# Kernel tuning notes

Measured on AMD Instinct MI355X. Metric: run time of the kernel, lower is better.

Reference implementation:

```python
import jax, jax.numpy as jnp
import numpy as np
import math

N_HEAD = 16
STRIDE = 128
C = 8


def _sparse_causal_mask(q_len, k_len):
    # Mirrors LingLongAttention._sparse_causal_mask (static, host-side numpy).
    cols = np.arange(k_len)
    rows = np.arange(k_len)[:, None]
    strided = (cols % STRIDE) >= (STRIDE - C)          # last C cols of each stride block
    local = (cols[None, :] // STRIDE) == (rows // STRIDE)  # same stride block as query
    causal = cols[None, :] <= rows
    layout = (strided[None, :] | local) & causal       # [k_len, k_len]
    return jnp.asarray(layout[k_len - q_len:])         # [q_len, k_len]


def setup_inputs() -> dict:
    key = jax.random.key(0)
    k1, k2, k3 = jax.random.split(key, 3)
    B, S, E = 2, 2048, 1024
    return {
        "hidden_states": jax.random.normal(k1, (B, S, E), dtype=jnp.float32),
        "W_attn": jax.random.normal(k2, (E, 3 * E), dtype=jnp.float32) * 0.02,
        "b_attn": jnp.zeros((3 * E,), dtype=jnp.float32),
        "W_proj": jax.random.normal(k3, (E, E), dtype=jnp.float32) * 0.02,
        "b_proj": jnp.zeros((E,), dtype=jnp.float32),
    }


def reference(hidden_states, W_attn, b_attn, W_proj, b_proj):
    B, S, E = hidden_states.shape
    H = N_HEAD
    D = E // H
    # Conv1D: x @ W + b, then split into q,k,v
    qkv = hidden_states @ W_attn + b_attn                 # [B,S,3E]
    q, k, v = jnp.split(qkv, 3, axis=-1)
    split = lambda t: t.reshape(B, S, H, D).transpose(0, 2, 1, 3)  # [B,H,S,D]
    q, k, v = split(q), split(k), split(v)
    scale = jnp.asarray(1.0 / math.sqrt(D), dtype=q.dtype)
    scores = jnp.einsum("bhqd,bhkd->bhqk", q, k) * scale  # [B,H,S,S]
    mask = _sparse_causal_mask(S, S)[None, None]          # [1,1,S,S]
    mask_value = jnp.asarray(jnp.finfo(scores.dtype).min, dtype=scores.dtype)
    scores = jnp.where(mask, scores, mask_value)
    attn = jax.nn.softmax(scores, axis=-1)
    out = jnp.einsum("bhqk,bhkd->bhqd", attn, v)          # [B,H,S,D]
    out = out.transpose(0, 2, 1, 3).reshape(B, S, E)      # merge heads
    return out @ W_proj + b_proj
```

## Files before the change

kernel.cpp:

```cpp
#include <hip/hip_runtime.h>
#include <hip/hip_bf16.h>
#include <stdint.h>

typedef unsigned short u16;
typedef uint32_t u32;
typedef short s16x8 __attribute__((ext_vector_type(8)));
typedef float f32x4 __attribute__((ext_vector_type(4)));

#define SDIM 2048
#define EDIM 1024

static __device__ __forceinline__ float b2f(u16 v) {
    union { float f; u32 u; } c; c.u = ((u32)v) << 16; return c.f;
}
static __device__ __forceinline__ u16 f2b(float f) {
    union { float f; u32 u; } c; c.f = f;
    u32 u = c.u;
    u32 r = (u + 0x7FFFu + ((u >> 16) & 1u)) >> 16;
    return (u16)r;
}
static __device__ __forceinline__ void gll16(const u16* g, u16* l) {
    __builtin_amdgcn_global_load_lds(
        (const __attribute__((address_space(1))) void*)g,
        (__attribute__((address_space(3))) void*)l, 16, 0, 0);
}

static __device__ __forceinline__ int sniff_bf16(const u16* __restrict__ x) {
    u16 v = x[(threadIdx.x & 63) * 2];
    int e = (v >> 7) & 0xFF;
    unsigned long long m = __ballot(e >= 90 && e <= 144);
    return __popcll(m) >= 48;
}

__global__ __launch_bounds__(256) void k_prep(
    const void* __restrict__ X, const void* __restrict__ Wa,
    const void* __restrict__ Wp, u16* __restrict__ Xb,
    u16* __restrict__ WtA, u16* __restrict__ WtP) {
    int f = sniff_bf16((const u16*)X);
    int z = blockIdx.z;
    int t = threadIdx.x;
    if (z == 2) {
        if (f) return;
        const float* s = (const float*)X;
        int bid = blockIdx.y * 48 + blockIdx.x;
        for (int c = bid; c < 2048; c += 768) {
            long i = ((long)c * 256 + t) * 8;
            u16 o[8];
            for (int j = 0; j < 8; ++j) o[j] = f2b(s[i + j]);
            *(uint4*)&Xb[i] = *(uint4*)o;
        }
        return;
    }
    if (z == 1 && blockIdx.x >= 16) return;
    const void* src = z ? Wp : Wa;
    u16* dst = z ? WtP : WtA;
    int Nsrc = z ? 1024 : 3072;
    int n0 = blockIdx.x * 64, k0 = blockIdx.y * 64;
    __shared__ u16 L[64 * 72];
    int r = t >> 2, c0 = (t & 3) * 16;
    u16 val[16];
    if (f) {
        const u16* s = (const u16*)src + (size_t)(k0 + r) * Nsrc + n0 + c0;
        *(uint4*)&val[0] = *(const uint4*)s;
        *(uint4*)&val[8] = *(const uint4*)(s + 8);
    } else {
        const float* s = (const float*)src + (size_t)(k0 + r) * Nsrc + n0 + c0;
        for (int j = 0; j < 16; ++j) val[j] = f2b(s[j]);
    }
    for (int j = 0; j < 16; ++j) L[(c0 + j) * 72 + r] = val[j];
    __syncthreads();
    uint4 o0 = *(const uint4*)&L[r * 72 + c0];
    uint4 o1 = *(const uint4*)&L[r * 72 + c0 + 8];
    u16* d = dst + (size_t)(n0 + r) * 1024 + k0 + c0;
    *(uint4*)d = o0;
    *(uint4*)(d + 8) = o1;
}

__global__ __launch_bounds__(256) void k_gemm1(
    const u16* __restrict__ Xraw, const u16* __restrict__ Xb,
    const u16* __restrict__ Bt, const void* __restrict__ bias,
    u16* __restrict__ C) {
    const int K = 1024, N = 3072;
    __shared__ u16 As[128 * 64];
    __shared__ u16 Bs[128 * 64];
    int f = sniff_bf16(Xraw);
    const u16* A = f ? Xraw : Xb;
    int t = threadIdx.x, wave = t >> 6, lane = t & 63;
    int m0 = blockIdx.y * 128, n0 = blockIdx.x * 128;
    int wm = (wave >> 1) * 64, wn = (wave & 1) * 64;
    int lm = lane & 15, lk = (lane >> 4) * 8;
    int sr = t >> 2, sc = (t & 3) * 8;
    const u16* Ap = A + (size_t)(m0 + sr) * K + sc;
    const u16* Bp = Bt + (size_t)(n0 + sr) * K + sc;
    u16* Asw = As + wave * 512;
    u16* Bsw = Bs + wave * 512;

    f32x4 acc[4][4];
    f32x4 z = {0.f, 0.f, 0.f, 0.f};
    for (int mi = 0; mi < 4; ++mi)
        for (int ni = 0; ni < 4; ++ni) acc[mi][ni] = z;

    for (int k0 = 0; k0 < K; k0 += 64) {
        gll16(Ap + k0, Asw);
        gll16(Ap + (size_t)64 * K + k0, Asw + 2048);
        gll16(Ap + k0 + 32, Asw + 4096);
        gll16(Ap + (size_t)64 * K + k0 + 32, Asw + 6144);
        gll16(Bp + k0, Bsw);
        gll16(Bp + (size_t)64 * K + k0, Bsw + 2048);
        gll16(Bp + k0 + 32, Bsw + 4096);
        gll16(Bp + (size_t)64 * K + k0 + 32, Bsw + 6144);
        __syncthreads();
        for (int kh = 0; kh < 2; ++kh) {
            const u16* Ab = As + kh * 4096;
            const u16* Bb = Bs + kh * 4096;
            s16x8 af[4], bfr[4];
            for (int mi = 0; mi < 4; ++mi)
                af[mi] = *(const s16x8*)&Ab[(wm + mi * 16 + lm) * 32 + lk];
            for (int ni = 0; ni < 4; ++ni)
                bfr[ni] = *(const s16x8*)&Bb[(wn + ni * 16 + lm) * 32 + lk];
            for (int mi = 0; mi < 4; ++mi)
                for (int ni = 0; ni < 4; ++ni)
                    acc[mi][ni] = __builtin_amdgcn_mfma_f32_16x16x32_bf16(
                        af[mi], bfr[ni], acc[mi][ni], 0, 0, 0);
        }
        __syncthreads();
    }

    int cn = lane & 15, cr = (lane >> 4) * 4;
    for (int ni = 0; ni < 4; ++ni) {
        int gn = n0 + wn + ni * 16 + cn;
        float bb = f ? b2f(((const u16*)bias)[gn]) : ((const float*)bias)[gn];
        for (int mi = 0; mi < 4; ++mi)
            for (int r = 0; r < 4; ++r) {
                int gm = m0 + wm + mi * 16 + cr + r;
                C[(size_t)gm * N + gn] = f2b(acc[mi][ni][r] + bb);
            }
    }
}

__global__ __launch_bounds__(256) void k_gemm2(
    const u16* __restrict__ Xraw, const u16* __restrict__ A,
    const u16* __restrict__ Bt, const void* __restrict__ bias,
    u16* __restrict__ Cb, float* __restrict__ Cf) {
    const int K = 1024, N = 1024;
    __shared__ u16 As[64 * 64];
    __shared__ u16 Bs[128 * 64];
    int f = sniff_bf16(Xraw);
    int t = threadIdx.x, wave = t >> 6, lane = t & 63;
    int m0 = blockIdx.y * 64, n0 = blockIdx.x * 128;
    int wm = (wave >> 1) * 32, wn = (wave & 1) * 64;
    int lm = lane & 15, lk = (lane >> 4) * 8;
    int sr = t >> 2, sc = (t & 3) * 8;
    const u16* Ap = A + (size_t)(m0 + sr) * K + sc;
    const u16* Bp = Bt + (size_t)(n0 + sr) * K + sc;
    u16* Asw = As + wave * 512;
    u16* Bsw = Bs + wave * 512;

    f32x4 acc[2][4];
    f32x4 z = {0.f, 0.f, 0.f, 0.f};
    for (int mi = 0; mi < 2; ++mi)
        for (int ni = 0; ni < 4; ++ni) acc[mi][ni] = z;

    for (int k0 = 0; k0 < K; k0 += 64) {
        gll16(Ap + k0, Asw);
        gll16(Ap + k0 + 32, Asw + 2048);
        gll16(Bp + k0, Bsw);
        gll16(Bp + (size_t)64 * K + k0, Bsw + 2048);
        gll16(Bp + k0 + 32, Bsw + 4096);
        gll16(Bp + (size_t)64 * K + k0 + 32, Bsw + 6144);
        __syncthreads();
        for (int kh = 0; kh < 2; ++kh) {
            const u16* Ab = As + kh * 2048;
            const u16* Bb = Bs + kh * 4096;
            s16x8 af[2], bfr[4];
            for (int mi = 0; mi < 2; ++mi)
                af[mi] = *(const s16x8*)&Ab[(wm + mi * 16 + lm) * 32 + lk];
            for (int ni = 0; ni < 4; ++ni)
                bfr[ni] = *(const s16x8*)&Bb[(wn + ni * 16 + lm) * 32 + lk];
            for (int mi = 0; mi < 2; ++mi)
                for (int ni = 0; ni < 4; ++ni)
                    acc[mi][ni] = __builtin_amdgcn_mfma_f32_16x16x32_bf16(
                        af[mi], bfr[ni], acc[mi][ni], 0, 0, 0);
        }
        __syncthreads();
    }

    int store_f32 = (f == 0);
    int cn = lane & 15, cr = (lane >> 4) * 4;
    for (int ni = 0; ni < 4; ++ni) {
        int gn = n0 + wn + ni * 16 + cn;
        float bb = f ? b2f(((const u16*)bias)[gn]) : ((const float*)bias)[gn];
        for (int mi = 0; mi < 2; ++mi)
            for (int r = 0; r < 4; ++r) {
                int gm = m0 + wm + mi * 16 + cr + r;
                float v = acc[mi][ni][r] + bb;
                size_t o = (size_t)gm * N + gn;
                if (store_f32) Cf[o] = v;
                else           Cb[o] = f2b(v);
            }
    }
}

#define VP 264
#define PP 264
__global__ __launch_bounds__(256) void k_attn3(const u16* __restrict__ QKV,
                                               u16* __restrict__ AO) {
    int bx = blockIdx.x, h = blockIdx.y, b = blockIdx.z;
    int qb = bx >> 1, sb = bx & 1;
    int t = threadIdx.x, lane = t & 63, wave = t >> 6;
    int lm = lane & 15, q4 = lane >> 4;
    int nstr = qb << 3;
    int nk = nstr + (sb << 6) + 64;
    int r0 = (qb << 7) + (sb << 6);

    __shared__ char smem[79872];
    u16* Vts = (u16*)smem;
    u16* Qs  = (u16*)(smem + 33792);
    u16* Ks  = (u16*)(smem + 33792 + 9216);
    u16* Ps  = (u16*)(smem + 33792);

    const u16* base = QKV + (size_t)b * SDIM * 3072;

    for (int c = t; c < 512; c += 256) {
        int r = c >> 3, d0 = (c & 7) << 3;
        *(uint4*)&Qs[r * 72 + d0] =
            *(const uint4*)(base + (size_t)(r0 + r) * 3072 + h * 64 + d0);
    }
    uint4 zz = {0u, 0u, 0u, 0u};
    for (int c = t; c < 2048; c += 256) {
        int i = c >> 3, d0 = (c & 7) << 3;
        uint4 kv = zz;
        if (i < nk) {
            int key = (i < nstr) ? (((i >> 3) << 7) + 120 + (i & 7))
                                 : ((qb << 7) + (i - nstr));
            kv = *(const uint4*)(base + (size_t)key * 3072 + 1024 + h * 64 + d0);
        }
        *(uint4*)&Ks[i * 72 + d0] = kv;
    }
    {
        int i0 = (t & 31) * 8, d0 = (t >> 5) * 8;
        u16 m8[8][8];
        for (int r = 0; r < 8; ++r) {
            int i = i0 + r;
            uint4 vv = zz;
            if (i < nk) {
                int key = (i < nstr) ? (((i >> 3) << 7) + 120 + (i & 7))
                                     : ((qb << 7) + (i - nstr));
                vv = *(const uint4*)(base + (size_t)key * 3072 + 2048 + h * 64 + d0);
            }
            *(uint4*)m8[r] = vv;
        }
        for (int j = 0; j < 8; ++j) {
            u16 o[8];
            for (int r = 0; r < 8; ++r) o[r] = m8[r][j];
            *(uint4*)&Vts[(d0 + j) * VP + i0] = *(uint4*)o;
        }
    }
    __syncthreads();

    f32x4 acc[16];
    f32x4 z4 = {0.f, 0.f, 0.f, 0.f};
    for (int ni = 0; ni < 16; ++ni) acc[ni] = z4;
    s16x8 af0 = *(const s16x8*)&Qs[(wave * 16 + lm) * 72 + q4 * 8];
    s16x8 af1 = *(const s16x8*)&Qs[(wave * 16 + lm) * 72 + 32 + q4 * 8];
    for (int ni = 0; ni < 16; ++ni) {
        s16x8 bf0 = *(const s16x8*)&Ks[(ni * 16 + lm) * 72 + q4 * 8];
        s16x8 bf1 = *(const s16x8*)&Ks[(ni * 16 + lm) * 72 + 32 + q4 * 8];
        acc[ni] = __builtin_amdgcn_mfma_f32_16x16x32_bf16(af0, bf0, acc[ni], 0, 0, 0);
        acc[ni] = __builtin_amdgcn_mfma_f32_16x16x32_bf16(af1, bf1, acc[ni], 0, 0, 0);
    }
    __syncthreads();

    float mx[4] = {-3e38f, -3e38f, -3e38f, -3e38f};
    for (int ni = 0; ni < 16; ++ni) {
        int i = ni * 16 + lm;
        for (int reg = 0; reg < 4; ++reg) {
            int rl = (sb << 6) + wave * 16 + q4 * 4 + reg;
            bool valid = (i < nstr) || ((i - nstr) <= rl);
            float v = valid ? acc[ni][reg] * 0.125f : -3e38f;
            acc[ni][reg] = v;
            mx[reg] = fmaxf(mx[reg], v);
        }
    }
    for (int reg = 0; reg < 4; ++reg)
        for (int off = 1; off < 16; off <<= 1)
            mx[reg] = fmaxf(mx[reg], __shfl_xor(mx[reg], off, 64));
    float sm[4] = {0.f, 0.f, 0.f, 0.f};
    for (int ni = 0; ni < 16; ++ni)
        for (int reg = 0; reg < 4; ++reg) {
            float e = __expf(acc[ni][reg] - mx[reg]);
            acc[ni][reg] = e;
            sm[reg] += e;
        }
    for (int reg = 0; reg < 4; ++reg)
        for (int off = 1; off < 16; off <<= 1)
            sm[reg] += __shfl_xor(sm[reg], off, 64);
    float inv[4];
    for (int reg = 0; reg < 4; ++reg) inv[reg] = 1.f / sm[reg];

    for (int ni = 0; ni < 16; ++ni) {
        int i = ni * 16 + lm;
        for (int reg = 0; reg < 4; ++reg)
            Ps[(wave * 16 + q4 * 4 + reg) * PP + i] = f2b(acc[ni][reg]);
    }
    __syncthreads();

    f32x4 acc2[4];
    for (int ni2 = 0; ni2 < 4; ++ni2) acc2[ni2] = z4;
    for (int k0 = 0; k0 < 256; k0 += 32) {
        s16x8 pf = *(const s16x8*)&Ps[(wave * 16 + lm) * PP + k0 + q4 * 8];
        for (int ni2 = 0; ni2 < 4; ++ni2) {
            s16x8 vf = *(const s16x8*)&Vts[(ni2 * 16 + lm) * VP + k0 + q4 * 8];
            acc2[ni2] = __builtin_amdgcn_mfma_f32_16x16x32_bf16(pf, vf, acc2[ni2], 0, 0, 0);
        }
    }
    int srow = r0 + wave * 16 + q4 * 4;
    for (int ni2 = 0; ni2 < 4; ++ni2)
        for (int reg = 0; reg < 4; ++reg) {
            size_t o = ((size_t)(b * SDIM + srow + reg)) * EDIM + h * 64 + ni2 * 16 + lm;
            AO[o] = f2b(acc2[ni2][reg] * inv[reg]);
        }
}

extern "C" void kernel_launch(void* const* d_in, const int* in_sizes, int n_in,
                              void* d_out, int out_size, void* d_ws, size_t ws_size,
                              hipStream_t stream) {
    const void* X  = d_in[0];
    const void* Wa = d_in[1];
    const void* ba = d_in[2];
    const void* Wp = d_in[3];
    const void* bp = d_in[4];

    char* w = (char*)d_ws;
    u16* Xb   = (u16*)(w);
    u16* WtA  = (u16*)(w + 8388608);
    u16* WtP  = (u16*)(w + 14680064);
    u16* QKV  = (u16*)(w + 16777216);
    u16* AO   = (u16*)(w + 41943040);

    k_prep<<<dim3(48, 16, 3), 256, 0, stream>>>(X, Wa, Wp, Xb, WtA, WtP);
    k_gemm1<<<dim3(24, 32), 256, 0, stream>>>((const u16*)X, Xb, WtA, ba, QKV);
    k_attn3<<<dim3(32, 16, 2), 256, 0, stream>>>(QKV, AO);
    k_gemm2<<<dim3(8, 64), 256, 0, stream>>>((const u16*)X, AO, WtP, bp,
                                             (u16*)d_out, (float*)d_out);
}
```

Baseline: 169.6 us.

## Double-buffer A tiles in LDS and load B fragments directly from global in GEMMs

Both projection GEMMs now double-buffer the A tile in shared memory and prefetch the next k-slice while the current one is computed. This leaves one barrier per iteration instead of two. The B operand is no longer staged through LDS; each wave reads its MFMA fragments straight from global memory into registers. This removes the B staging and LDS traffic, but B is now fetched redundantly by the two waves that share a column range. The direct global loads also sit in the critical path with no prefetch distance, and they raise register pressure.

```diff
diff --git a/kernel.cpp b/kernel.cpp
--- a/kernel.cpp
+++ b/kernel.cpp
@@ -81,8 +81,7 @@
     const u16* __restrict__ Bt, const void* __restrict__ bias,
     u16* __restrict__ C) {
     const int K = 1024, N = 3072;
-    __shared__ u16 As[128 * 64];
-    __shared__ u16 Bs[128 * 64];
+    __shared__ u16 As[2 * 8192];
     int f = sniff_bf16(Xraw);
     const u16* A = f ? Xraw : Xb;
     int t = threadIdx.x, wave = t >> 6, lane = t & 63;
@@ -91,37 +90,44 @@
     int lm = lane & 15, lk = (lane >> 4) * 8;
     int sr = t >> 2, sc = (t & 3) * 8;
     const u16* Ap = A + (size_t)(m0 + sr) * K + sc;
-    const u16* Bp = Bt + (size_t)(n0 + sr) * K + sc;
-    u16* Asw = As + wave * 512;
-    u16* Bsw = Bs + wave * 512;
+    const u16* Bl = Bt + (size_t)(n0 + wn + lm) * K + lk;
+    u16* Asw0 = As + wave * 512;
 
     f32x4 acc[4][4];
     f32x4 z = {0.f, 0.f, 0.f, 0.f};
     for (int mi = 0; mi < 4; ++mi)
         for (int ni = 0; ni < 4; ++ni) acc[mi][ni] = z;
 
-    for (int k0 = 0; k0 < K; k0 += 64) {
-        gll16(Ap + k0, Asw);
-        gll16(Ap + (size_t)64 * K + k0, Asw + 2048);
-        gll16(Ap + k0 + 32, Asw + 4096);
-        gll16(Ap + (size_t)64 * K + k0 + 32, Asw + 6144);
-        gll16(Bp + k0, Bsw);
-        gll16(Bp + (size_t)64 * K + k0, Bsw + 2048);
-        gll16(Bp + k0 + 32, Bsw + 4096);
-        gll16(Bp + (size_t)64 * K + k0 + 32, Bsw + 6144);
-        __syncthreads();
+    gll16(Ap, Asw0);
+    gll16(Ap + (size_t)64 * K, Asw0 + 2048);
+    gll16(Ap + 32, Asw0 + 4096);
+    gll16(Ap + (size_t)64 * K + 32, Asw0 + 6144);
+    __syncthreads();
+
+    for (int it = 0; it < 16; ++it) {
+        int k0 = it * 64;
+        const u16* cur = As + (it & 1) * 8192;
+        if (it < 15) {
+            u16* nxt = As + ((it + 1) & 1) * 8192 + wave * 512;
+            int kn = k0 + 64;
+            gll16(Ap + kn, nxt);
+            gll16(Ap + (size_t)64 * K + kn, nxt + 2048);
+            gll16(Ap + kn + 32, nxt + 4096);
+            gll16(Ap + (size_t)64 * K + kn + 32, nxt + 6144);
+        }
+        s16x8 bfr[2][4];
+        for (int kh = 0; kh < 2; ++kh)
+            for (int ni = 0; ni < 4; ++ni)
+                bfr[kh][ni] = *(const s16x8*)(Bl + (size_t)(ni * 16) * K + k0 + kh * 32);
         for (int kh = 0; kh < 2; ++kh) {
-            const u16* Ab = As + kh * 4096;
-            const u16* Bb = Bs + kh * 4096;
-            s16x8 af[4], bfr[4];
+            const u16* Ab = cur + kh * 4096;
+            s16x8 af[4];
             for (int mi = 0; mi < 4; ++mi)
                 af[mi] = *(const s16x8*)&Ab[(wm + mi * 16 + lm) * 32 + lk];
-            for (int ni = 0; ni < 4; ++ni)
-                bfr[ni] = *(const s16x8*)&Bb[(wn + ni * 16 + lm) * 32 + lk];
             for (int mi = 0; mi < 4; ++mi)
                 for (int ni = 0; ni < 4; ++ni)
                     acc[mi][ni] = __builtin_amdgcn_mfma_f32_16x16x32_bf16(
-                        af[mi], bfr[ni], acc[mi][ni], 0, 0, 0);
+                        af[mi], bfr[kh][ni], acc[mi][ni], 0, 0, 0);
         }
         __syncthreads();
     }
@@ -143,8 +149,7 @@
     const u16* __restrict__ Bt, const void* __restrict__ bias,
     u16* __restrict__ Cb, float* __restrict__ Cf) {
     const int K = 1024, N = 1024;
-    __shared__ u16 As[64 * 64];
-    __shared__ u16 Bs[128 * 64];
+    __shared__ u16 As[2 * 4096];
     int f = sniff_bf16(Xraw);
     int t = threadIdx.x, wave = t >> 6, lane = t & 63;
     int m0 = blockIdx.y * 64, n0 = blockIdx.x * 128;
@@ -152,35 +157,40 @@
     int lm = lane & 15, lk = (lane >> 4) * 8;
     int sr = t >> 2, sc = (t & 3) * 8;
     const u16* Ap = A + (size_t)(m0 + sr) * K + sc;
-    const u16* Bp = Bt + (size_t)(n0 + sr) * K + sc;
-    u16* Asw = As + wave * 512;
-    u16* Bsw = Bs + wave * 512;
+    const u16* Bl = Bt + (size_t)(n0 + wn + lm) * K + lk;
+    u16* Asw0 = As + wave * 512;
 
     f32x4 acc[2][4];
     f32x4 z = {0.f, 0.f, 0.f, 0.f};
     for (int mi = 0; mi < 2; ++mi)
         for (int ni = 0; ni < 4; ++ni) acc[mi][ni] = z;
 
-    for (int k0 = 0; k0 < K; k0 += 64) {
-        gll16(Ap + k0, Asw);
-        gll16(Ap + k0 + 32, Asw + 2048);
-        gll16(Bp + k0, Bsw);
-        gll16(Bp + (size_t)64 * K + k0, Bsw + 2048);
-        gll16(Bp + k0 + 32, Bsw + 4096);
-        gll16(Bp + (size_t)64 * K + k0 + 32, Bsw + 6144);
-        __syncthreads();
+    gll16(Ap, Asw0);
+    gll16(Ap + 32, Asw0 + 2048);
+    __syncthreads();
+
+    for (int it = 0; it < 16; ++it) {
+        int k0 = it * 64;
+        const u16* cur = As + (it & 1) * 4096;
+        if (it < 15) {
+            u16* nxt = As + ((it + 1) & 1) * 4096 + wave * 512;
+            int kn = k0 + 64;
+            gll16(Ap + kn, nxt);
+            gll16(Ap + kn + 32, nxt + 2048);
+        }
+        s16x8 bfr[2][4];
+        for (int kh = 0; kh < 2; ++kh)
+            for (int ni = 0; ni < 4; ++ni)
+                bfr[kh][ni] = *(const s16x8*)(Bl + (size_t)(ni * 16) * K + k0 + kh * 32);
         for (int kh = 0; kh < 2; ++kh) {
-            const u16* Ab = As + kh * 2048;
-            const u16* Bb = Bs + kh * 4096;
-            s16x8 af[2], bfr[4];
+            const u16* Ab = cur + kh * 2048;
+            s16x8 af[2];
             for (int mi = 0; mi < 2; ++mi)
                 af[mi] = *(const s16x8*)&Ab[(wm + mi * 16 + lm) * 32 + lk];
-            for (int ni = 0; ni < 4; ++ni)
-                bfr[ni] = *(const s16x8*)&Bb[(wn + ni * 16 + lm) * 32 + lk];
             for (int mi = 0; mi < 2; ++mi)
                 for (int ni = 0; ni < 4; ++ni)
                     acc[mi][ni] = __builtin_amdgcn_mfma_f32_16x16x32_bf16(
-                        af[mi], bfr[ni], acc[mi][ni], 0, 0, 0);
+                        af[mi], bfr[kh][ni], acc[mi][ni], 0, 0, 0);
         }
         __syncthreads();
     }
```

After: 219.5 us. 29.4% more time.

## Load QKV GEMM fragments directly from global memory with register double-buffering

Applied to the files above, without the earlier changes.

The QKV projection GEMM no longer stages A and B tiles through LDS with barriers. Each wave now loads its MFMA operand fragments straight from global memory into registers, using two fragment sets so the next k-step's loads are in flight while the current one computes. This removes LDS traffic and __syncthreads stalls, but it also drops sharing of tiles between waves: each row is read from global/L2 by two waves, and the extra fragment set raises register pressure.

```diff
diff --git a/kernel.cpp b/kernel.cpp
--- a/kernel.cpp
+++ b/kernel.cpp
@@ -76,54 +76,52 @@
     *(uint4*)(d + 8) = o1;
 }
 
+struct Frag { s16x8 a[2][4]; s16x8 b[2][4]; };
+
+static __device__ __forceinline__ void ldfrag(
+    Frag& fr, const u16* __restrict__ Al, const u16* __restrict__ Bl,
+    int k0, const int K) {
+    for (int kh = 0; kh < 2; ++kh) {
+        for (int mi = 0; mi < 4; ++mi)
+            fr.a[kh][mi] = *(const s16x8*)(Al + (size_t)(mi * 16) * K + k0 + kh * 32);
+        for (int ni = 0; ni < 4; ++ni)
+            fr.b[kh][ni] = *(const s16x8*)(Bl + (size_t)(ni * 16) * K + k0 + kh * 32);
+    }
+}
+static __device__ __forceinline__ void cmpfrag(f32x4 acc[4][4], const Frag& fr) {
+    for (int kh = 0; kh < 2; ++kh)
+        for (int mi = 0; mi < 4; ++mi)
+            for (int ni = 0; ni < 4; ++ni)
+                acc[mi][ni] = __builtin_amdgcn_mfma_f32_16x16x32_bf16(
+                    fr.a[kh][mi], fr.b[kh][ni], acc[mi][ni], 0, 0, 0);
+}
+
 __global__ __launch_bounds__(256) void k_gemm1(
     const u16* __restrict__ Xraw, const u16* __restrict__ Xb,
     const u16* __restrict__ Bt, const void* __restrict__ bias,
     u16* __restrict__ C) {
     const int K = 1024, N = 3072;
-    __shared__ u16 As[128 * 64];
-    __shared__ u16 Bs[128 * 64];
     int f = sniff_bf16(Xraw);
     const u16* A = f ? Xraw : Xb;
     int t = threadIdx.x, wave = t >> 6, lane = t & 63;
     int m0 = blockIdx.y * 128, n0 = blockIdx.x * 128;
     int wm = (wave >> 1) * 64, wn = (wave & 1) * 64;
     int lm = lane & 15, lk = (lane >> 4) * 8;
-    int sr = t >> 2, sc = (t & 3) * 8;
-    const u16* Ap = A + (size_t)(m0 + sr) * K + sc;
-    const u16* Bp = Bt + (size_t)(n0 + sr) * K + sc;
-    u16* Asw = As + wave * 512;
-    u16* Bsw = Bs + wave * 512;
+    const u16* Al = A + (size_t)(m0 + wm + lm) * K + lk;
+    const u16* Bl = Bt + (size_t)(n0 + wn + lm) * K + lk;
 
     f32x4 acc[4][4];
     f32x4 z = {0.f, 0.f, 0.f, 0.f};
     for (int mi = 0; mi < 4; ++mi)
         for (int ni = 0; ni < 4; ++ni) acc[mi][ni] = z;
 
-    for (int k0 = 0; k0 < K; k0 += 64) {
-        gll16(Ap + k0, Asw);
-        gll16(Ap + (size_t)64 * K + k0, Asw + 2048);
-        gll16(Ap + k0 + 32, Asw + 4096);
-        gll16(Ap + (size_t)64 * K + k0 + 32, Asw + 6144);
-        gll16(Bp + k0, Bsw);
-        gll16(Bp + (size_t)64 * K + k0, Bsw + 2048);
-        gll16(Bp + k0 + 32, Bsw + 4096);
-        gll16(Bp + (size_t)64 * K + k0 + 32, Bsw + 6144);
-        __syncthreads();
-        for (int kh = 0; kh < 2; ++kh) {
-            const u16* Ab = As + kh * 4096;
-            const u16* Bb = Bs + kh * 4096;
-            s16x8 af[4], bfr[4];
-            for (int mi = 0; mi < 4; ++mi)
-                af[mi] = *(const s16x8*)&Ab[(wm + mi * 16 + lm) * 32 + lk];
-            for (int ni = 0; ni < 4; ++ni)
-                bfr[ni] = *(const s16x8*)&Bb[(wn + ni * 16 + lm) * 32 + lk];
-            for (int mi = 0; mi < 4; ++mi)
-                for (int ni = 0; ni < 4; ++ni)
-                    acc[mi][ni] = __builtin_amdgcn_mfma_f32_16x16x32_bf16(
-                        af[mi], bfr[ni], acc[mi][ni], 0, 0, 0);
-        }
-        __syncthreads();
+    Frag f0, f1;
+    ldfrag(f0, Al, Bl, 0, K);
+    for (int it = 0; it < 16; it += 2) {
+        ldfrag(f1, Al, Bl, (it + 1) * 64, K);
+        cmpfrag(acc, f0);
+        if (it + 2 < 16) ldfrag(f0, Al, Bl, (it + 2) * 64, K);
+        cmpfrag(acc, f1);
     }
 
     int cn = lane & 15, cr = (lane >> 4) * 4;
```

After: 228.7 us. 1.35x slower.
